# Optimization experiments

Hardware: AMD Instinct MI355X
Metric: run time of the kernel (lower is better)

## Reference

```python
import jax, jax.numpy as jnp
import numpy as np

N_HEAD = 16
MASK_SCALE = 10000.0  # matches torch buffer construction


def setup_inputs() -> dict:
    key = jax.random.key(0)
    k1, k2 = jax.random.split(key)
    B, T, C = 2, 2048, 1024
    x = jax.random.normal(k1, (B, T, C), dtype=jnp.float32)
    # packed q,k projection: nn.Linear(C, 2C, bias=False) -> weight [2C, C]
    W_attn = jax.random.normal(k2, (2 * C, C), dtype=jnp.float32) * 0.02
    alpha = jnp.array(1.0, dtype=jnp.float32)
    beta = jnp.array(0.1, dtype=jnp.float32)
    gamma = jnp.array(0.1, dtype=jnp.float32)
    return {"x": x, "W_attn": W_attn, "alpha": alpha, "beta": beta, "gamma": gamma}


def _shaped_attention(x, W_attn, alpha, beta, gamma):
    B, T, C = x.shape
    H = N_HEAD
    hd = C // H
    # packed projection then split into q, k (use_v=False -> v comes from x)
    qk = jnp.einsum('btc,oc->bto', x, W_attn)  # [B,T,2C]
    q, k = jnp.split(qk, 2, axis=-1)
    q = q.reshape(B, T, H, hd).transpose(0, 2, 1, 3)  # [B,H,T,hd]
    k = k.reshape(B, T, H, hd).transpose(0, 2, 1, 3)
    v = x.reshape(B, T, H, hd).transpose(0, 2, 1, 3)

    scores = jnp.einsum('bhqd,bhkd->bhqk', q, k) * (hd ** -0.5)
    tril = jnp.tril(jnp.ones((T, T), dtype=bool))
    scores = jnp.where(tril, scores, -jnp.inf)
    att = jax.nn.softmax(scores, axis=-1)  # [B,H,T,T]

    # fixed structured masks, built exactly as the torch buffers
    Id = jax.nn.softmax(jnp.eye(T, dtype=jnp.float32) * MASK_SCALE, axis=-1)
    MC = jax.nn.softmax(tril.astype(jnp.float32) * MASK_SCALE, axis=-1)

    shaped = beta * att + alpha * Id[None, None] - gamma * MC[None, None]
    y = jnp.einsum('bhqk,bhkd->bhqd', shaped, v)
    return y.transpose(0, 2, 1, 3).reshape(B, T, C)  # c_proj is Identity


def reference(x, W_attn, alpha, beta, gamma):
    return _shaped_attention(x, W_attn, alpha, beta, gamma)
```

## Files before the change

kernel.cpp:

```cpp
#include <hip/hip_runtime.h>
#include <hip/hip_bf16.h>

typedef __attribute__((ext_vector_type(8))) short bf16x8;
typedef __attribute__((ext_vector_type(4))) float f32x4;
typedef unsigned short u16;

#define B_  2
#define T_  2048
#define C_  1024
#define H_  16
#define HD_ 64

static __device__ __forceinline__ u16 f2bf(float f) {
  unsigned u = __float_as_uint(f);
  u += 0x7fffu + ((u >> 16) & 1u);
  return (u16)(u >> 16);
}

#define NX4 1048576
#define NW4 524288
__global__ __launch_bounds__(256) void prep(
    const float* __restrict__ X, const float* __restrict__ W,
    u16* __restrict__ Xb, u16* __restrict__ Wb,
    u16* __restrict__ Vf, float* __restrict__ SubP)
{
  __shared__ u16 tr[64][65];
  const int blk = blockIdx.x;
  const int tid = threadIdx.x;

  if (blk < 6144) {
    int i = blk * 256 + tid;
    if (i < NX4) {
      float4 v = ((const float4*)X)[i];
      ushort4 u = { f2bf(v.x), f2bf(v.y), f2bf(v.z), f2bf(v.w) };
      ((ushort4*)Xb)[i] = u;
    } else {
      int j = i - NX4;
      float4 v = ((const float4*)W)[j];
      ushort4 u = { f2bf(v.x), f2bf(v.y), f2bf(v.z), f2bf(v.w) };
      ((ushort4*)Wb)[j] = u;
    }
  } else if (blk < 6144 + 1024) {
    int idx = blk - 6144;
    const int kt = idx & 31, bh = idx >> 5;
    const int b = bh >> 4, h = bh & 15;
    {
      const int row = tid >> 2;
      const int c0  = (tid & 3) * 16;
      const float* xp = X + ((size_t)b * T_ + kt * 64 + row) * C_ + h * 64 + c0;
#pragma unroll
      for (int q = 0; q < 4; ++q) {
        float4 v = *(const float4*)(xp + q * 4);
        tr[row][c0 + q * 4 + 0] = f2bf(v.x);
        tr[row][c0 + q * 4 + 1] = f2bf(v.y);
        tr[row][c0 + q * 4 + 2] = f2bf(v.z);
        tr[row][c0 + q * 4 + 3] = f2bf(v.w);
      }
    }
    __syncthreads();
    const int w = tid >> 6, lane = tid & 63, quad = (lane >> 4), l16 = lane & 15;
    u16* outb = Vf + ((size_t)bh * 32 + kt) * 4096;
#pragma unroll
    for (int c = 0; c < 2; ++c) {
      u16 tmp[8];
#pragma unroll
      for (int j = 0; j < 8; ++j) tmp[j] = tr[c * 32 + quad * 8 + j][w * 16 + l16];
      *(bf16x8*)&outb[((w * 2 + c) * 64 + lane) * 8] = *(const bf16x8*)tmp;
    }
  } else {
    int idx = blk - 7168;
    const int ch = idx & 15, bh = idx >> 4;
    const int b = bh >> 4, h = bh & 15;
    const int d = tid & 63, s = tid >> 6;
    const float* xp = X + (size_t)b * T_ * C_ + h * 64 + d;
    int t0 = ch * 128 + s * 32;
    float sum = 0.f;
#pragma unroll 8
    for (int i = 0; i < 32; ++i) sum += xp[(size_t)(t0 + i) * C_];
    SubP[((size_t)bh * 64 + ch * 4 + s) * 64 + d] = sum;
  }
}

__global__ __launch_bounds__(256) void gemm_qk(
    const u16* __restrict__ Xb, const u16* __restrict__ Wb,
    u16* __restrict__ Qo, u16* __restrict__ Kf)
{
  __shared__ __align__(16) u16 As[128 * 64];
  __shared__ __align__(16) u16 Bs[128 * 64];

  const int tid  = threadIdx.x;
  const int w    = tid >> 6;
  const int lane = tid & 63;
  const int quad = lane >> 4;
  const int l16  = lane & 15;
  const int m0 = blockIdx.y * 128;
  const int n0 = blockIdx.x * 128;

  const int grow = w * 8 + ((lane >> 3) & 7);
  const int gcol = (lane & 7) * 8;

  f32x4 zero = {0.f, 0.f, 0.f, 0.f};
  f32x4 acc[4][4];
#pragma unroll
  for (int i = 0; i < 4; ++i)
#pragma unroll
    for (int j = 0; j < 4; ++j) acc[i][j] = zero;

  const int wr = (w >> 1) * 64, wc = (w & 1) * 64;

  for (int k0 = 0; k0 < C_; k0 += 64) {
#pragma unroll
    for (int r = 0; r < 4; ++r) {
      const u16* ga = Xb + (size_t)(m0 + grow + r * 32) * C_ + k0 + gcol;
      const u16* gb = Wb + (size_t)(n0 + grow + r * 32) * C_ + k0 + gcol;
      __builtin_amdgcn_global_load_lds(
          (const __attribute__((address_space(1))) void*)ga,
          (__attribute__((address_space(3))) void*)&As[(w * 8 + r * 32) * 64],
          16, 0, 0);
      __builtin_amdgcn_global_load_lds(
          (const __attribute__((address_space(1))) void*)gb,
          (__attribute__((address_space(3))) void*)&Bs[(w * 8 + r * 32) * 64],
          16, 0, 0);
    }
    __syncthreads();
#pragma unroll
    for (int c = 0; c < 2; ++c) {
      bf16x8 af[4], bf[4];
#pragma unroll
      for (int i = 0; i < 4; ++i)
        af[i] = *(const bf16x8*)&As[(wr + i * 16 + l16) * 64 + c * 32 + quad * 8];
#pragma unroll
      for (int j = 0; j < 4; ++j)
        bf[j] = *(const bf16x8*)&Bs[(wc + j * 16 + l16) * 64 + c * 32 + quad * 8];
#pragma unroll
      for (int i = 0; i < 4; ++i)
#pragma unroll
        for (int j = 0; j < 4; ++j)
          acc[i][j] = __builtin_amdgcn_mfma_f32_16x16x32_bf16(af[i], bf[j], acc[i][j], 0, 0, 0);
    }
    __syncthreads();
  }

#pragma unroll
  for (int i = 0; i < 4; ++i) {
#pragma unroll
    for (int j = 0; j < 4; ++j) {
      int n = n0 + wc + j * 16 + l16;
      if (n < C_) {
        int h = n >> 6, d = n & 63;
#pragma unroll
        for (int r = 0; r < 4; ++r) {
          int m = m0 + wr + i * 16 + quad * 4 + r;
          int b = m >> 11, t = m & (T_ - 1);
          Qo[(((size_t)b * H_ + h) * T_ + t) * HD_ + d] = f2bf(acc[i][j][r]);
        }
      } else {
        int nh = n - C_;
        int hh = nh >> 6, d = nh & 63;
#pragma unroll
        for (int r = 0; r < 4; ++r) {
          int m = m0 + wr + i * 16 + quad * 4 + r;
          int b = m >> 11, t = m & (T_ - 1);
          int bh = b * H_ + hh;
          size_t idx = (((((size_t)bh * 32 + (t >> 6)) * 4 + ((t >> 4) & 3)) * 2
                         + (d >> 5)) * 64 + ((d >> 3) & 3) * 16 + (t & 15)) * 8
                       + (d & 7);
          Kf[idx] = f2bf(acc[i][j][r]);
        }
      }
    }
  }
}

__device__ __forceinline__ void load_kv(
    bf16x8 (&kf)[2][4], bf16x8 (&vf)[2][4],
    const u16* __restrict__ kbase, const u16* __restrict__ vbase, int lane)
{
#pragma unroll
  for (int c = 0; c < 2; ++c)
#pragma unroll
    for (int nb = 0; nb < 4; ++nb) {
      kf[c][nb] = *(const bf16x8*)&kbase[((nb * 2 + c) * 64 + lane) * 8];
      vf[c][nb] = *(const bf16x8*)&vbase[((nb * 2 + c) * 64 + lane) * 8];
    }
}

__device__ __forceinline__ void tile_compute(
    const bf16x8 (&qfrag)[2], const bf16x8 (&kf)[2][4], const bf16x8 (&vf)[2][4],
    f32x4 (&acc)[4], f32x4& accl, float (*pb)[68],
    int quad, int l16, int myrow, bool diag, bf16x8 onesf)
{
  f32x4 zero = {0.f, 0.f, 0.f, 0.f};
  f32x4 sfr[4] = {zero, zero, zero, zero};
#pragma unroll
  for (int cc = 0; cc < 2; ++cc)
#pragma unroll
    for (int nb = 0; nb < 4; ++nb)
      sfr[nb] = __builtin_amdgcn_mfma_f32_16x16x32_bf16(qfrag[cc], kf[cc][nb], sfr[nb], 0, 0, 0);

#pragma unroll
  for (int nb = 0; nb < 4; ++nb)
#pragma unroll
    for (int r = 0; r < 4; ++r) {
      float p = __expf(sfr[nb][r] * 0.125f);
      if (diag && (nb * 16 + l16 > myrow + r)) p = 0.f;
      pb[quad * 4 + r][nb * 16 + l16] = p;
    }

#pragma unroll
  for (int cc = 0; cc < 2; ++cc) {
    f32x4 plo = *(const f32x4*)&pb[l16][cc * 32 + quad * 8];
    f32x4 phi = *(const f32x4*)&pb[l16][cc * 32 + quad * 8 + 4];
    union { unsigned u[4]; bf16x8 v; } pk;
    __hip_bfloat162 hh;
    hh = __float22bfloat162_rn(make_float2(plo[0], plo[1])); pk.u[0] = *(unsigned*)&hh;
    hh = __float22bfloat162_rn(make_float2(plo[2], plo[3])); pk.u[1] = *(unsigned*)&hh;
    hh = __float22bfloat162_rn(make_float2(phi[0], phi[1])); pk.u[2] = *(unsigned*)&hh;
    hh = __float22bfloat162_rn(make_float2(phi[2], phi[3])); pk.u[3] = *(unsigned*)&hh;
    accl = __builtin_amdgcn_mfma_f32_16x16x32_bf16(pk.v, onesf, accl, 0, 0, 0);
#pragma unroll
    for (int nb = 0; nb < 4; ++nb)
      acc[nb] = __builtin_amdgcn_mfma_f32_16x16x32_bf16(pk.v, vf[cc][nb], acc[nb], 0, 0, 0);
  }
}

__global__ __launch_bounds__(256) void attn_kernel(
    const u16* __restrict__ Q, const u16* __restrict__ Kf, const u16* __restrict__ Vf,
    const float* __restrict__ SubP, const float* __restrict__ X, float* __restrict__ out,
    const float* __restrict__ alphap, const float* __restrict__ betap,
    const float* __restrict__ gammap)
{
  __shared__ __align__(16) char smem[19456];

  const int tid  = threadIdx.x;
  const int w    = tid >> 6;
  const int lane = tid & 63;
  const int quad = lane >> 4;
  const int l16  = lane & 15;
  const int qt = 31 - blockIdx.y;
  const int bh = blockIdx.x;
  const int b = bh >> 4, h = bh & 15;

  const u16* qb  = Q  + (size_t)bh * T_ * HD_;
  const u16* kfb = Kf + (size_t)bh * T_ * HD_;
  const u16* vfb = Vf + (size_t)bh * T_ * HD_;

  bf16x8 qfrag[2];
  {
    const u16* qp = qb + (size_t)(qt * 64 + w * 16 + l16) * HD_ + quad * 8;
    qfrag[0] = *(const bf16x8*)qp;
    qfrag[1] = *(const bf16x8*)(qp + 32);
  }

  bf16x8 onesf;
#pragma unroll
  for (int j = 0; j < 8; ++j) onesf[j] = (short)0x3F80;

  f32x4 zero = {0.f, 0.f, 0.f, 0.f};
  f32x4 acc[4] = {zero, zero, zero, zero};
  f32x4 accl = zero;
  const int myrow = w * 16 + quad * 4;
  float (*pb)[68] = (float(*)[68])((float*)smem + (size_t)w * 16 * 68);

  bf16x8 kA[2][4], vA[2][4], kB[2][4], vB[2][4];
  load_kv(kA, vA, kfb, vfb, lane);
  int kt = 0;
  for (;;) {
    int ktn = (kt + 1 < qt) ? kt + 1 : qt;
    load_kv(kB, vB, kfb + (size_t)ktn * 4096, vfb + (size_t)ktn * 4096, lane);
    tile_compute(qfrag, kA, vA, acc, accl, pb, quad, l16, myrow, kt == qt, onesf);
    if (kt + 1 > qt) break;
    int ktn2 = (kt + 2 < qt) ? kt + 2 : qt;
    load_kv(kA, vA, kfb + (size_t)ktn2 * 4096, vfb + (size_t)ktn2 * 4096, lane);
    tile_compute(qfrag, kB, vB, acc, accl, pb, quad, l16, myrow, kt + 1 == qt, onesf);
    kt += 2;
    if (kt > qt) break;
  }

  __syncthreads();
  float* Xt = (float*)smem;
  float* G  = (float*)(smem + 17408);
  float* GP = (float*)(smem + 18432);

  {
    const int row = tid >> 2, c0 = (tid & 3) * 16;
    const float* xp = X + ((size_t)b * T_ + qt * 64 + row) * C_ + h * 64 + c0;
#pragma unroll
    for (int q = 0; q < 4; ++q) {
      float4 v = *(const float4*)(xp + q * 4);
      Xt[row * 68 + c0 + q * 4 + 0] = v.x;
      Xt[row * 68 + c0 + q * 4 + 1] = v.y;
      Xt[row * 68 + c0 + q * 4 + 2] = v.z;
      Xt[row * 68 + c0 + q * 4 + 3] = v.w;
    }
  }
  {
    float p = 0.f;
    for (int i = w; i < 2 * qt; i += 4)
      p += SubP[(size_t)bh * 4096 + i * 64 + lane];
    GP[w * 64 + lane] = p;
  }
  __syncthreads();
  {
    float g = 0.f;
#pragma unroll
    for (int i = 0; i < 16; ++i) g += Xt[(w * 16 + i) * 68 + lane];
    G[w * 64 + lane] = g;
  }
  __syncthreads();
  {
    const float alpha = *alphap, gamma = *gammap;
    float run = GP[lane] + GP[64 + lane] + GP[128 + lane] + GP[192 + lane];
    for (int g = 0; g < w; ++g) run += G[g * 64 + lane];
    const int tbase = qt * 64 + w * 16;
#pragma unroll
    for (int i = 0; i < 16; ++i) {
      float v = Xt[(w * 16 + i) * 68 + lane];
      run += v;
      Xt[(w * 16 + i) * 68 + lane] =
          alpha * v - gamma * run * __builtin_amdgcn_rcpf((float)(tbase + i + 1));
    }
  }
  __syncthreads();

  const float beta = *betap;
  float rl[4];
#pragma unroll
  for (int r = 0; r < 4; ++r) rl[r] = beta * __builtin_amdgcn_rcpf(accl[r]);
#pragma unroll
  for (int nb = 0; nb < 4; ++nb) {
#pragma unroll
    for (int r = 0; r < 4; ++r) {
      int t = qt * 64 + myrow + r;
      int d = nb * 16 + l16;
      out[((size_t)b * T_ + t) * C_ + h * 64 + d] =
          Xt[(myrow + r) * 68 + d] + rl[r] * acc[nb][r];
    }
  }
}

extern "C" void kernel_launch(void* const* d_in, const int* in_sizes, int n_in,
                              void* d_out, int out_size, void* d_ws, size_t ws_size,
                              hipStream_t stream) {
  const float* x      = (const float*)d_in[0];
  const float* W_attn = (const float*)d_in[1];
  const float* alphap = (const float*)d_in[2];
  const float* betap  = (const float*)d_in[3];
  const float* gammap = (const float*)d_in[4];
  float* out = (float*)d_out;

  char* ws = (char*)d_ws;
  u16*   Qb   = (u16*)(ws);
  u16*   Kfb  = (u16*)(ws + (8ull  << 20));
  u16*   Vfb  = (u16*)(ws + (16ull << 20));
  float* SubP = (float*)(ws + (24ull << 20));
  u16*   Xb   = (u16*)(ws + (25ull << 20));
  u16*   Wb   = (u16*)(ws + (33ull << 20));

  prep<<<7680, 256, 0, stream>>>(x, W_attn, Xb, Wb, Vfb, SubP);
  gemm_qk<<<dim3(16, 32), 256, 0, stream>>>(Xb, Wb, Qb, Kfb);
  attn_kernel<<<dim3(32, 32), 256, 0, stream>>>(Qb, Kfb, Vfb, SubP, x, out,
                                                alphap, betap, gammap);
}
```

Measured before the change: 156.1 us.

## Split attention KV tiles across two waves per 16-row block with hierarchical prefix sums

The attention kernel now launches one 128-thread block per 16 query rows, replacing one 256-thread block per 64 rows. The two waves in a block take alternating KV tiles and merge their partial accumulators through shared memory. The causal-mean term is rebuilt from precomputed 16-row and 128-row column partial sums plus in-wave shuffles, replacing the shared-memory scan over the whole X tile. The score scale is folded into Q during the GEMM epilogue, and the K/Q stores are simplified. The aim is finer load balancing across the causal triangle and a shorter serial KV loop per wave. In exchange, each block re-reads its Q fragments, and the split adds a shared-memory reduction and another prefix-sum buffer.

```diff
diff --git a/kernel.cpp b/kernel.cpp
--- a/kernel.cpp
+++ b/kernel.cpp
@@ -22,9 +22,9 @@
 __global__ __launch_bounds__(256) void prep(
     const float* __restrict__ X, const float* __restrict__ W,
     u16* __restrict__ Xb, u16* __restrict__ Wb,
-    u16* __restrict__ Vf, float* __restrict__ SubP)
+    u16* __restrict__ Vf, float* __restrict__ SubP16, float* __restrict__ SubP128)
 {
-  __shared__ u16 tr[64][65];
+  __shared__ __align__(16) char shb[8320];
   const int blk = blockIdx.x;
   const int tid = threadIdx.x;
 
@@ -40,7 +40,8 @@
       ushort4 u = { f2bf(v.x), f2bf(v.y), f2bf(v.z), f2bf(v.w) };
       ((ushort4*)Wb)[j] = u;
     }
-  } else if (blk < 6144 + 1024) {
+  } else if (blk < 7168) {
+    u16 (*tr)[65] = (u16(*)[65])shb;
     int idx = blk - 6144;
     const int kt = idx & 31, bh = idx >> 5;
     const int b = bh >> 4, h = bh & 15;
@@ -68,16 +69,25 @@
       *(bf16x8*)&outb[((w * 2 + c) * 64 + lane) * 8] = *(const bf16x8*)tmp;
     }
   } else {
+    float* cs = (float*)shb;
     int idx = blk - 7168;
     const int ch = idx & 15, bh = idx >> 4;
     const int b = bh >> 4, h = bh & 15;
     const int d = tid & 63, s = tid >> 6;
     const float* xp = X + (size_t)b * T_ * C_ + h * 64 + d;
     int t0 = ch * 128 + s * 32;
-    float sum = 0.f;
-#pragma unroll 8
-    for (int i = 0; i < 32; ++i) sum += xp[(size_t)(t0 + i) * C_];
-    SubP[((size_t)bh * 64 + ch * 4 + s) * 64 + d] = sum;
+    float sa = 0.f, sb = 0.f;
+#pragma unroll 4
+    for (int i = 0; i < 16; ++i) sa += xp[(size_t)(t0 + i) * C_];
+#pragma unroll 4
+    for (int i = 16; i < 32; ++i) sb += xp[(size_t)(t0 + i) * C_];
+    SubP16[((size_t)bh * 128 + ch * 8 + s * 2) * 64 + d] = sa;
+    SubP16[((size_t)bh * 128 + ch * 8 + s * 2 + 1) * 64 + d] = sb;
+    cs[s * 64 + d] = sa + sb;
+    __syncthreads();
+    if (s == 0)
+      SubP128[((size_t)bh * 16 + ch) * 64 + d] =
+          cs[d] + cs[64 + d] + cs[128 + d] + cs[192 + d];
   }
 }
 
@@ -143,30 +153,25 @@
 
 #pragma unroll
   for (int i = 0; i < 4; ++i) {
+    const int t_base = m0 + wr + i * 16;
+    const int bidx = t_base >> 11;
+    const int kt   = (t_base & 2047) >> 6;
+    const int trow = (t_base & 2047) + quad * 4;
 #pragma unroll
     for (int j = 0; j < 4; ++j) {
-      int n = n0 + wc + j * 16 + l16;
+      const int n = n0 + wc + j * 16 + l16;
       if (n < C_) {
-        int h = n >> 6, d = n & 63;
-#pragma unroll
-        for (int r = 0; r < 4; ++r) {
-          int m = m0 + wr + i * 16 + quad * 4 + r;
-          int b = m >> 11, t = m & (T_ - 1);
-          Qo[(((size_t)b * H_ + h) * T_ + t) * HD_ + d] = f2bf(acc[i][j][r]);
-        }
+        const int hq = n >> 6, d = n & 63;
+        u16* qp = Qo + (((size_t)bidx * H_ + hq) * T_ + trow) * HD_ + d;
+#pragma unroll
+        for (int r = 0; r < 4; ++r) qp[(size_t)r * HD_] = f2bf(0.125f * acc[i][j][r]);
       } else {
-        int nh = n - C_;
-        int hh = nh >> 6, d = nh & 63;
-#pragma unroll
-        for (int r = 0; r < 4; ++r) {
-          int m = m0 + wr + i * 16 + quad * 4 + r;
-          int b = m >> 11, t = m & (T_ - 1);
-          int bh = b * H_ + hh;
-          size_t idx = (((((size_t)bh * 32 + (t >> 6)) * 4 + ((t >> 4) & 3)) * 2
-                         + (d >> 5)) * 64 + ((d >> 3) & 3) * 16 + (t & 15)) * 8
-                       + (d & 7);
-          Kf[idx] = f2bf(acc[i][j][r]);
-        }
+        const int nh = n - C_;
+        const int hh = nh >> 6, d = nh & 63;
+        u16* kp = Kf + (((((size_t)(bidx * H_ + hh) * 32 + kt) * 4 + i) * 2 + (d >> 5)) * 64
+                        + ((d >> 3) & 3) * 16 + quad * 4) * 8 + (d & 7);
+#pragma unroll
+        for (int r = 0; r < 4; ++r) kp[(size_t)r * 8] = f2bf(acc[i][j][r]);
       }
     }
   }
@@ -188,7 +193,7 @@
 __device__ __forceinline__ void tile_compute(
     const bf16x8 (&qfrag)[2], const bf16x8 (&kf)[2][4], const bf16x8 (&vf)[2][4],
     f32x4 (&acc)[4], f32x4& accl, float (*pb)[68],
-    int quad, int l16, int myrow, bool diag, bf16x8 onesf)
+    int quad, int l16, int wrow, bool diag, bf16x8 onesf)
 {
   f32x4 zero = {0.f, 0.f, 0.f, 0.f};
   f32x4 sfr[4] = {zero, zero, zero, zero};
@@ -198,14 +203,22 @@
     for (int nb = 0; nb < 4; ++nb)
       sfr[nb] = __builtin_amdgcn_mfma_f32_16x16x32_bf16(qfrag[cc], kf[cc][nb], sfr[nb], 0, 0, 0);
 
-#pragma unroll
-  for (int nb = 0; nb < 4; ++nb)
-#pragma unroll
-    for (int r = 0; r < 4; ++r) {
-      float p = __expf(sfr[nb][r] * 0.125f);
-      if (diag && (nb * 16 + l16 > myrow + r)) p = 0.f;
-      pb[quad * 4 + r][nb * 16 + l16] = p;
-    }
+  if (diag) {
+#pragma unroll
+    for (int nb = 0; nb < 4; ++nb)
+#pragma unroll
+      for (int r = 0; r < 4; ++r) {
+        float p = __expf(sfr[nb][r]);
+        if (nb * 16 + l16 > wrow + quad * 4 + r) p = 0.f;
+        pb[quad * 4 + r][nb * 16 + l16] = p;
+      }
+  } else {
+#pragma unroll
+    for (int nb = 0; nb < 4; ++nb)
+#pragma unroll
+      for (int r = 0; r < 4; ++r)
+        pb[quad * 4 + r][nb * 16 + l16] = __expf(sfr[nb][r]);
+  }
 
 #pragma unroll
   for (int cc = 0; cc < 2; ++cc) {
@@ -224,30 +237,34 @@
   }
 }
 
-__global__ __launch_bounds__(256) void attn_kernel(
+__global__ __launch_bounds__(128) void attn_kernel(
     const u16* __restrict__ Q, const u16* __restrict__ Kf, const u16* __restrict__ Vf,
-    const float* __restrict__ SubP, const float* __restrict__ X, float* __restrict__ out,
+    const float* __restrict__ SubP16, const float* __restrict__ SubP128,
+    const float* __restrict__ X, float* __restrict__ out,
     const float* __restrict__ alphap, const float* __restrict__ betap,
     const float* __restrict__ gammap)
 {
-  __shared__ __align__(16) char smem[19456];
+  __shared__ __align__(16) float pbs[2][16][68];
+  __shared__ float redl[16];
 
   const int tid  = threadIdx.x;
-  const int w    = tid >> 6;
+  const int p    = tid >> 6;
   const int lane = tid & 63;
   const int quad = lane >> 4;
   const int l16  = lane & 15;
   const int qt = 31 - blockIdx.y;
+  const int w  = blockIdx.z;
   const int bh = blockIdx.x;
   const int b = bh >> 4, h = bh & 15;
-
-  const u16* qb  = Q  + (size_t)bh * T_ * HD_;
+  const int wrow  = w * 16;
+  const int qrow0 = qt * 64 + wrow;
+
   const u16* kfb = Kf + (size_t)bh * T_ * HD_;
   const u16* vfb = Vf + (size_t)bh * T_ * HD_;
 
   bf16x8 qfrag[2];
   {
-    const u16* qp = qb + (size_t)(qt * 64 + w * 16 + l16) * HD_ + quad * 8;
+    const u16* qp = Q + ((size_t)bh * T_ + qrow0 + l16) * HD_ + quad * 8;
     qfrag[0] = *(const bf16x8*)qp;
     qfrag[1] = *(const bf16x8*)(qp + 32);
   }
@@ -259,82 +276,101 @@
   f32x4 zero = {0.f, 0.f, 0.f, 0.f};
   f32x4 acc[4] = {zero, zero, zero, zero};
   f32x4 accl = zero;
-  const int myrow = w * 16 + quad * 4;
-  float (*pb)[68] = (float(*)[68])((float*)smem + (size_t)w * 16 * 68);
-
-  bf16x8 kA[2][4], vA[2][4], kB[2][4], vB[2][4];
-  load_kv(kA, vA, kfb, vfb, lane);
-  int kt = 0;
-  for (;;) {
-    int ktn = (kt + 1 < qt) ? kt + 1 : qt;
-    load_kv(kB, vB, kfb + (size_t)ktn * 4096, vfb + (size_t)ktn * 4096, lane);
-    tile_compute(qfrag, kA, vA, acc, accl, pb, quad, l16, myrow, kt == qt, onesf);
-    if (kt + 1 > qt) break;
-    int ktn2 = (kt + 2 < qt) ? kt + 2 : qt;
-    load_kv(kA, vA, kfb + (size_t)ktn2 * 4096, vfb + (size_t)ktn2 * 4096, lane);
-    tile_compute(qfrag, kB, vB, acc, accl, pb, quad, l16, myrow, kt + 1 == qt, onesf);
-    kt += 2;
-    if (kt > qt) break;
-  }
-
+  float (*pb)[68] = pbs[p];
+
+  const bool hasDiag = ((qt & 1) == p);
+  const int n = (qt - p + 1) >> 1;
+  const int total = n + (hasDiag ? 1 : 0);
+
+  if (total > 0) {
+    const int D = total - 1;
+    bf16x8 kA[2][4], vA[2][4], kB[2][4], vB[2][4];
+    int k0 = (0 < n) ? p : qt;
+    load_kv(kA, vA, kfb + (size_t)k0 * 4096, vfb + (size_t)k0 * 4096, lane);
+    int i = 0;
+    while (i + 2 <= D) {
+      int k1 = (i + 1 < n) ? p + 2 * (i + 1) : qt;
+      load_kv(kB, vB, kfb + (size_t)k1 * 4096, vfb + (size_t)k1 * 4096, lane);
+      tile_compute(qfrag, kA, vA, acc, accl, pb, quad, l16, wrow, false, onesf);
+      int k2 = (i + 2 < n) ? p + 2 * (i + 2) : qt;
+      load_kv(kA, vA, kfb + (size_t)k2 * 4096, vfb + (size_t)k2 * 4096, lane);
+      tile_compute(qfrag, kB, vB, acc, accl, pb, quad, l16, wrow, false, onesf);
+      i += 2;
+    }
+    if (i < D) {
+      int k1 = (i + 1 < n) ? p + 2 * (i + 1) : qt;
+      load_kv(kB, vB, kfb + (size_t)k1 * 4096, vfb + (size_t)k1 * 4096, lane);
+      tile_compute(qfrag, kA, vA, acc, accl, pb, quad, l16, wrow, false, onesf);
+      tile_compute(qfrag, kB, vB, acc, accl, pb, quad, l16, wrow, hasDiag, onesf);
+    } else {
+      tile_compute(qfrag, kA, vA, acc, accl, pb, quad, l16, wrow, hasDiag, onesf);
+    }
+  }
+
+  if (p == 1) {
+#pragma unroll
+    for (int nb = 0; nb < 4; ++nb)
+#pragma unroll
+      for (int r = 0; r < 4; ++r)
+        pbs[1][quad * 4 + r][nb * 16 + l16] = acc[nb][r];
+    if (l16 == 0) {
+#pragma unroll
+      for (int r = 0; r < 4; ++r) redl[quad * 4 + r] = accl[r];
+    }
+  }
   __syncthreads();
-  float* Xt = (float*)smem;
-  float* G  = (float*)(smem + 17408);
-  float* GP = (float*)(smem + 18432);
-
-  {
-    const int row = tid >> 2, c0 = (tid & 3) * 16;
-    const float* xp = X + ((size_t)b * T_ + qt * 64 + row) * C_ + h * 64 + c0;
-#pragma unroll
-    for (int q = 0; q < 4; ++q) {
-      float4 v = *(const float4*)(xp + q * 4);
-      Xt[row * 68 + c0 + q * 4 + 0] = v.x;
-      Xt[row * 68 + c0 + q * 4 + 1] = v.y;
-      Xt[row * 68 + c0 + q * 4 + 2] = v.z;
-      Xt[row * 68 + c0 + q * 4 + 3] = v.w;
-    }
-  }
-  {
-    float p = 0.f;
-    for (int i = w; i < 2 * qt; i += 4)
-      p += SubP[(size_t)bh * 4096 + i * 64 + lane];
-    GP[w * 64 + lane] = p;
-  }
-  __syncthreads();
-  {
-    float g = 0.f;
-#pragma unroll
-    for (int i = 0; i < 16; ++i) g += Xt[(w * 16 + i) * 68 + lane];
-    G[w * 64 + lane] = g;
-  }
-  __syncthreads();
-  {
-    const float alpha = *alphap, gamma = *gammap;
-    float run = GP[lane] + GP[64 + lane] + GP[128 + lane] + GP[192 + lane];
-    for (int g = 0; g < w; ++g) run += G[g * 64 + lane];
-    const int tbase = qt * 64 + w * 16;
-#pragma unroll
-    for (int i = 0; i < 16; ++i) {
-      float v = Xt[(w * 16 + i) * 68 + lane];
-      run += v;
-      Xt[(w * 16 + i) * 68 + lane] =
-          alpha * v - gamma * run * __builtin_amdgcn_rcpf((float)(tbase + i + 1));
-    }
-  }
-  __syncthreads();
-
-  const float beta = *betap;
+  if (p == 1) return;
+
+#pragma unroll
+  for (int nb = 0; nb < 4; ++nb)
+#pragma unroll
+    for (int r = 0; r < 4; ++r)
+      acc[nb][r] += pbs[1][quad * 4 + r][nb * 16 + l16];
+#pragma unroll
+  for (int r = 0; r < 4; ++r) accl[r] += redl[quad * 4 + r];
+
+  float xv[4][4];
+  const float* xb = X + ((size_t)b * T_ + qrow0) * C_ + h * 64;
+#pragma unroll
+  for (int nb = 0; nb < 4; ++nb)
+#pragma unroll
+    for (int r = 0; r < 4; ++r)
+      xv[nb][r] = xb[(size_t)(quad * 4 + r) * C_ + nb * 16 + l16];
+
+  const int g16 = qt * 4 + w;
+  float base[4];
+#pragma unroll
+  for (int nb = 0; nb < 4; ++nb) {
+    float loc = xv[nb][0] + xv[nb][1] + xv[nb][2] + xv[nb][3];
+    float p1 = __shfl(loc, (lane - 16) & 63);
+    float p2 = __shfl(loc, (lane - 32) & 63);
+    float p3 = __shfl(loc, (lane - 48) & 63);
+    float e = 0.f;
+    if (quad > 0) e += p1;
+    if (quad > 1) e += p2;
+    if (quad > 2) e += p3;
+    const int col = nb * 16 + l16;
+    const float* p128 = SubP128 + (size_t)bh * 16 * 64 + col;
+    const float* p16  = SubP16  + (size_t)bh * 128 * 64 + col;
+    for (int j = 0; j < (g16 >> 3); ++j) e += p128[(size_t)j * 64];
+    for (int k = g16 & ~7; k < g16; ++k) e += p16[(size_t)k * 64];
+    base[nb] = e;
+  }
+
+  const float alpha = *alphap, beta = *betap, gamma = *gammap;
   float rl[4];
 #pragma unroll
   for (int r = 0; r < 4; ++r) rl[r] = beta * __builtin_amdgcn_rcpf(accl[r]);
 #pragma unroll
   for (int nb = 0; nb < 4; ++nb) {
+    float run = base[nb];
 #pragma unroll
     for (int r = 0; r < 4; ++r) {
-      int t = qt * 64 + myrow + r;
-      int d = nb * 16 + l16;
-      out[((size_t)b * T_ + t) * C_ + h * 64 + d] =
-          Xt[(myrow + r) * 68 + d] + rl[r] * acc[nb][r];
+      run += xv[nb][r];
+      int t = qrow0 + quad * 4 + r;
+      out[((size_t)b * T_ + t) * C_ + h * 64 + nb * 16 + l16] =
+          alpha * xv[nb][r] - gamma * run * __builtin_amdgcn_rcpf((float)(t + 1))
+          + rl[r] * acc[nb][r];
     }
   }
 }
@@ -350,15 +386,16 @@
   float* out = (float*)d_out;
 
   char* ws = (char*)d_ws;
-  u16*   Qb   = (u16*)(ws);
-  u16*   Kfb  = (u16*)(ws + (8ull  << 20));
-  u16*   Vfb  = (u16*)(ws + (16ull << 20));
-  float* SubP = (float*)(ws + (24ull << 20));
-  u16*   Xb   = (u16*)(ws + (25ull << 20));
-  u16*   Wb   = (u16*)(ws + (33ull << 20));
-
-  prep<<<7680, 256, 0, stream>>>(x, W_attn, Xb, Wb, Vfb, SubP);
+  u16*   Qb    = (u16*)(ws);
+  u16*   Kfb   = (u16*)(ws + (8ull  << 20));
+  u16*   Vfb   = (u16*)(ws + (16ull << 20));
+  float* SubP16  = (float*)(ws + (24ull << 20));
+  float* SubP128 = (float*)(ws + (25ull << 20));
+  u16*   Xb    = (u16*)(ws + (26ull << 20));
+  u16*   Wb    = (u16*)(ws + (34ull << 20));
+
+  prep<<<7680, 256, 0, stream>>>(x, W_attn, Xb, Wb, Vfb, SubP16, SubP128);
   gemm_qk<<<dim3(16, 32), 256, 0, stream>>>(Xb, Wb, Qb, Kfb);
-  attn_kernel<<<dim3(32, 32), 256, 0, stream>>>(Qb, Kfb, Vfb, SubP, x, out,
-                                                alphap, betap, gammap);
-}
+  attn_kernel<<<dim3(32, 32, 4), 128, 0, stream>>>(Qb, Kfb, Vfb, SubP16, SubP128,
+                                                   x, out, alphap, betap, gammap);
+}
```

Result: slower. 171.9 us (+10.2%).

## Fuse X conversion, V transpose and column sums into one prep pass

Applied to the files above, without the earlier changes.

The prep kernel now reads each X tile once and, from that single read, writes the bf16 X copy, the transposed V fragments and per-64-row column sums (via shuffle reduction). This removes the separate X conversion blocks and the strided column-sum pass that each re-read X. The softmax scale is also folded into Q at the GEMM epilogue, and the Q/K store index math is hoisted out of the inner loops. The attention prefix-sum loop now reads half as many partial sums.

```diff
diff --git a/kernel.cpp b/kernel.cpp
--- a/kernel.cpp
+++ b/kernel.cpp
@@ -17,67 +17,73 @@
   return (u16)(u >> 16);
 }
 
-#define NX4 1048576
 #define NW4 524288
 __global__ __launch_bounds__(256) void prep(
     const float* __restrict__ X, const float* __restrict__ W,
     u16* __restrict__ Xb, u16* __restrict__ Wb,
-    u16* __restrict__ Vf, float* __restrict__ SubP)
+    u16* __restrict__ Vf, float* __restrict__ SubP64)
 {
   __shared__ u16 tr[64][65];
+  __shared__ float cs[4][64];
   const int blk = blockIdx.x;
   const int tid = threadIdx.x;
 
-  if (blk < 6144) {
-    int i = blk * 256 + tid;
-    if (i < NX4) {
-      float4 v = ((const float4*)X)[i];
-      ushort4 u = { f2bf(v.x), f2bf(v.y), f2bf(v.z), f2bf(v.w) };
-      ((ushort4*)Xb)[i] = u;
-    } else {
-      int j = i - NX4;
-      float4 v = ((const float4*)W)[j];
-      ushort4 u = { f2bf(v.x), f2bf(v.y), f2bf(v.z), f2bf(v.w) };
-      ((ushort4*)Wb)[j] = u;
-    }
-  } else if (blk < 6144 + 1024) {
-    int idx = blk - 6144;
-    const int kt = idx & 31, bh = idx >> 5;
+  if (blk < 1024) {
+    const int kt = blk & 31, bh = blk >> 5;
     const int b = bh >> 4, h = bh & 15;
+    const int w = tid >> 6, lane = tid & 63;
     {
       const int row = tid >> 2;
       const int c0  = (tid & 3) * 16;
       const float* xp = X + ((size_t)b * T_ + kt * 64 + row) * C_ + h * 64 + c0;
+      float vals[16];
 #pragma unroll
       for (int q = 0; q < 4; ++q) {
         float4 v = *(const float4*)(xp + q * 4);
-        tr[row][c0 + q * 4 + 0] = f2bf(v.x);
-        tr[row][c0 + q * 4 + 1] = f2bf(v.y);
-        tr[row][c0 + q * 4 + 2] = f2bf(v.z);
-        tr[row][c0 + q * 4 + 3] = f2bf(v.w);
+        vals[q * 4 + 0] = v.x; vals[q * 4 + 1] = v.y;
+        vals[q * 4 + 2] = v.z; vals[q * 4 + 3] = v.w;
       }
+      u16 xb[16];
+#pragma unroll
+      for (int i = 0; i < 16; ++i) xb[i] = f2bf(vals[i]);
+      u16* xq = Xb + ((size_t)(b * T_ + kt * 64 + row)) * C_ + h * 64 + c0;
+      *(bf16x8*)xq       = *(const bf16x8*)&xb[0];
+      *(bf16x8*)(xq + 8) = *(const bf16x8*)&xb[8];
+#pragma unroll
+      for (int i = 0; i < 16; ++i) tr[row][c0 + i] = xb[i];
+#pragma unroll
+      for (int m = 4; m <= 32; m <<= 1)
+#pragma unroll
+        for (int i = 0; i < 16; ++i) vals[i] += __shfl_xor(vals[i], m);
+      if (lane < 4) {
+        float* dst = &cs[w][lane * 16];
+#pragma unroll
+        for (int q = 0; q < 4; ++q) {
+          f32x4 s4 = { vals[q * 4 + 0], vals[q * 4 + 1], vals[q * 4 + 2], vals[q * 4 + 3] };
+          *(f32x4*)&dst[q * 4] = s4;
+        }
+      }
     }
     __syncthreads();
-    const int w = tid >> 6, lane = tid & 63, quad = (lane >> 4), l16 = lane & 15;
-    u16* outb = Vf + ((size_t)bh * 32 + kt) * 4096;
-#pragma unroll
-    for (int c = 0; c < 2; ++c) {
-      u16 tmp[8];
-#pragma unroll
-      for (int j = 0; j < 8; ++j) tmp[j] = tr[c * 32 + quad * 8 + j][w * 16 + l16];
-      *(bf16x8*)&outb[((w * 2 + c) * 64 + lane) * 8] = *(const bf16x8*)tmp;
-    }
+    {
+      const int quad = (lane >> 4), l16 = lane & 15;
+      u16* outb = Vf + ((size_t)bh * 32 + kt) * 4096;
+#pragma unroll
+      for (int c = 0; c < 2; ++c) {
+        u16 tmp[8];
+#pragma unroll
+        for (int j = 0; j < 8; ++j) tmp[j] = tr[c * 32 + quad * 8 + j][w * 16 + l16];
+        *(bf16x8*)&outb[((w * 2 + c) * 64 + lane) * 8] = *(const bf16x8*)tmp;
+      }
+    }
+    if (tid < 64)
+      SubP64[(size_t)bh * 2048 + kt * 64 + tid] =
+          cs[0][tid] + cs[1][tid] + cs[2][tid] + cs[3][tid];
   } else {
-    int idx = blk - 7168;
-    const int ch = idx & 15, bh = idx >> 4;
-    const int b = bh >> 4, h = bh & 15;
-    const int d = tid & 63, s = tid >> 6;
-    const float* xp = X + (size_t)b * T_ * C_ + h * 64 + d;
-    int t0 = ch * 128 + s * 32;
-    float sum = 0.f;
-#pragma unroll 8
-    for (int i = 0; i < 32; ++i) sum += xp[(size_t)(t0 + i) * C_];
-    SubP[((size_t)bh * 64 + ch * 4 + s) * 64 + d] = sum;
+    int i = (blk - 1024) * 256 + tid;
+    float4 v = ((const float4*)W)[i];
+    ushort4 u = { f2bf(v.x), f2bf(v.y), f2bf(v.z), f2bf(v.w) };
+    ((ushort4*)Wb)[i] = u;
   }
 }
 
@@ -143,30 +149,25 @@
 
 #pragma unroll
   for (int i = 0; i < 4; ++i) {
+    const int t_base = m0 + wr + i * 16;
+    const int bidx = t_base >> 11;
+    const int kt   = (t_base & 2047) >> 6;
+    const int trow = (t_base & 2047) + quad * 4;
 #pragma unroll
     for (int j = 0; j < 4; ++j) {
-      int n = n0 + wc + j * 16 + l16;
+      const int n = n0 + wc + j * 16 + l16;
       if (n < C_) {
-        int h = n >> 6, d = n & 63;
-#pragma unroll
-        for (int r = 0; r < 4; ++r) {
-          int m = m0 + wr + i * 16 + quad * 4 + r;
-          int b = m >> 11, t = m & (T_ - 1);
-          Qo[(((size_t)b * H_ + h) * T_ + t) * HD_ + d] = f2bf(acc[i][j][r]);
-        }
+        const int hq = n >> 6, d = n & 63;
+        u16* qp = Qo + (((size_t)bidx * H_ + hq) * T_ + trow) * HD_ + d;
+#pragma unroll
+        for (int r = 0; r < 4; ++r) qp[(size_t)r * HD_] = f2bf(0.125f * acc[i][j][r]);
       } else {
-        int nh = n - C_;
-        int hh = nh >> 6, d = nh & 63;
-#pragma unroll
-        for (int r = 0; r < 4; ++r) {
-          int m = m0 + wr + i * 16 + quad * 4 + r;
-          int b = m >> 11, t = m & (T_ - 1);
-          int bh = b * H_ + hh;
-          size_t idx = (((((size_t)bh * 32 + (t >> 6)) * 4 + ((t >> 4) & 3)) * 2
-                         + (d >> 5)) * 64 + ((d >> 3) & 3) * 16 + (t & 15)) * 8
-                       + (d & 7);
-          Kf[idx] = f2bf(acc[i][j][r]);
-        }
+        const int nh = n - C_;
+        const int hh = nh >> 6, d = nh & 63;
+        u16* kp = Kf + (((((size_t)(bidx * H_ + hh) * 32 + kt) * 4 + i) * 2 + (d >> 5)) * 64
+                        + ((d >> 3) & 3) * 16 + quad * 4) * 8 + (d & 7);
+#pragma unroll
+        for (int r = 0; r < 4; ++r) kp[(size_t)r * 8] = f2bf(acc[i][j][r]);
       }
     }
   }
@@ -202,7 +203,7 @@
   for (int nb = 0; nb < 4; ++nb)
 #pragma unroll
     for (int r = 0; r < 4; ++r) {
-      float p = __expf(sfr[nb][r] * 0.125f);
+      float p = __expf(sfr[nb][r]);
       if (diag && (nb * 16 + l16 > myrow + r)) p = 0.f;
       pb[quad * 4 + r][nb * 16 + l16] = p;
     }
@@ -226,7 +227,7 @@
 
 __global__ __launch_bounds__(256) void attn_kernel(
     const u16* __restrict__ Q, const u16* __restrict__ Kf, const u16* __restrict__ Vf,
-    const float* __restrict__ SubP, const float* __restrict__ X, float* __restrict__ out,
+    const float* __restrict__ SubP64, const float* __restrict__ X, float* __restrict__ out,
     const float* __restrict__ alphap, const float* __restrict__ betap,
     const float* __restrict__ gammap)
 {
@@ -241,13 +242,12 @@
   const int bh = blockIdx.x;
   const int b = bh >> 4, h = bh & 15;
 
-  const u16* qb  = Q  + (size_t)bh * T_ * HD_;
   const u16* kfb = Kf + (size_t)bh * T_ * HD_;
   const u16* vfb = Vf + (size_t)bh * T_ * HD_;
 
   bf16x8 qfrag[2];
   {
-    const u16* qp = qb + (size_t)(qt * 64 + w * 16 + l16) * HD_ + quad * 8;
+    const u16* qp = Q + ((size_t)bh * T_ + qt * 64 + w * 16 + l16) * HD_ + quad * 8;
     qfrag[0] = *(const bf16x8*)qp;
     qfrag[1] = *(const bf16x8*)(qp + 32);
   }
@@ -296,8 +296,8 @@
   }
   {
     float p = 0.f;
-    for (int i = w; i < 2 * qt; i += 4)
-      p += SubP[(size_t)bh * 4096 + i * 64 + lane];
+    for (int i = w; i < qt; i += 4)
+      p += SubP64[(size_t)bh * 2048 + i * 64 + lane];
     GP[w * 64 + lane] = p;
   }
   __syncthreads();
@@ -350,15 +350,15 @@
   float* out = (float*)d_out;
 
   char* ws = (char*)d_ws;
-  u16*   Qb   = (u16*)(ws);
-  u16*   Kfb  = (u16*)(ws + (8ull  << 20));
-  u16*   Vfb  = (u16*)(ws + (16ull << 20));
-  float* SubP = (float*)(ws + (24ull << 20));
-  u16*   Xb   = (u16*)(ws + (25ull << 20));
-  u16*   Wb   = (u16*)(ws + (33ull << 20));
-
-  prep<<<7680, 256, 0, stream>>>(x, W_attn, Xb, Wb, Vfb, SubP);
+  u16*   Qb     = (u16*)(ws);
+  u16*   Kfb    = (u16*)(ws + (8ull  << 20));
+  u16*   Vfb    = (u16*)(ws + (16ull << 20));
+  float* SubP64 = (float*)(ws + (24ull << 20));
+  u16*   Xb     = (u16*)(ws + (25ull << 20));
+  u16*   Wb     = (u16*)(ws + (33ull << 20));
+
+  prep<<<3072, 256, 0, stream>>>(x, W_attn, Xb, Wb, Vfb, SubP64);
   gemm_qk<<<dim3(16, 32), 256, 0, stream>>>(Xb, Wb, Qb, Kfb);
-  attn_kernel<<<dim3(32, 32), 256, 0, stream>>>(Qb, Kfb, Vfb, SubP, x, out,
+  attn_kernel<<<dim3(32, 32), 256, 0, stream>>>(Qb, Kfb, Vfb, SubP64, x, out,
                                                 alphap, betap, gammap);
 }
```

New measurement: 151.8 us. 1.03x faster.
